# Kernel tuning notes

Hardware: AMD Instinct MI355X
Metric: run time of the kernel (lower is better)

## Reference

```python
import jax, jax.numpy as jnp
import numpy as np

NUM_HEADS = 8
ALPHA = 0.01  # leaky_relu slope
MAX_SEQ = 64


def layer_norm(x, g, b, eps=1e-5):
    m = jnp.mean(x, axis=-1, keepdims=True)
    v = jnp.var(x, axis=-1, keepdims=True)
    return (x - m) * jax.lax.rsqrt(v + eps) * g + b


def ff(x, w1, b1, w2, b2):
    # Linear -> exact GELU -> Linear (torch nn.GELU default is erf-based)
    return jax.nn.gelu(x @ w1.T + b1, approximate=False) @ w2.T + b2


def mha(q, k, v, in_w, in_b, out_w, out_b, kpm):
    # torch nn.MultiheadAttention, batch_first=False. q:[Tq,E,d], k/v:[Tk,E,d], kpm:[E,Tk] True=pad
    d = q.shape[-1]
    H = NUM_HEADS
    dh = d // H
    qp = q @ in_w[:d].T + in_b[:d]
    kp = k @ in_w[d:2 * d].T + in_b[d:2 * d]
    vp = v @ in_w[2 * d:].T + in_b[2 * d:]
    Tq, E, _ = qp.shape
    Tk = kp.shape[0]
    qh = qp.reshape(Tq, E, H, dh) * (dh ** -0.5)
    kh = kp.reshape(Tk, E, H, dh)
    vh = vp.reshape(Tk, E, H, dh)
    scores = jnp.einsum('qehd,kehd->ehqk', qh, kh)  # [E,H,Tq,Tk]
    scores = jnp.where(kpm[:, None, None, :], jnp.float32(-1e9), scores)
    att = jax.nn.softmax(scores, axis=-1)
    out = jnp.einsum('ehqk,kehd->qehd', att, vh).reshape(Tq, E, d)
    return out @ out_w.T + out_b


def setup_inputs() -> dict:
    key = jax.random.key(0)
    ks = jax.random.split(key, 40)
    N, d, E, Seq, H = 50000, 64, 150000, 5, NUM_HEADS

    def xn(k, shape, scale):
        return jax.random.normal(k, shape, dtype=jnp.float32) * scale

    inp = {
        'features': xn(ks[0], (N, d), 1.0),
        'pos_emb': xn(ks[1], (MAX_SEQ, d), 0.02),
        'self_in_w': xn(ks[2], (3 * d, d), 0.1),
        'self_in_b': jnp.zeros((3 * d,), jnp.float32),
        'self_out_w': xn(ks[3], (d, d), 0.1),
        'self_out_b': jnp.zeros((d,), jnp.float32),
        'cross_in_w': xn(ks[4], (3 * d, d), 0.1),
        'cross_in_b': jnp.zeros((3 * d,), jnp.float32),
        'cross_out_w': xn(ks[5], (d, d), 0.1),
        'cross_out_b': jnp.zeros((d,), jnp.float32),
        'sa_ln1_g': jnp.ones((d,), jnp.float32), 'sa_ln1_b': jnp.zeros((d,), jnp.float32),
        'sa_ln2_g': jnp.ones((d,), jnp.float32), 'sa_ln2_b': jnp.zeros((d,), jnp.float32),
        'ca_ln1_g': jnp.ones((d,), jnp.float32), 'ca_ln1_b': jnp.zeros((d,), jnp.float32),
        'ca_ln2_g': jnp.ones((d,), jnp.float32), 'ca_ln2_b': jnp.zeros((d,), jnp.float32),
        'sa_ff_w1': xn(ks[6], (4 * d, d), 0.08), 'sa_ff_b1': jnp.zeros((4 * d,), jnp.float32),
        'sa_ff_w2': xn(ks[7], (d, 4 * d), 0.08), 'sa_ff_b2': jnp.zeros((d,), jnp.float32),
        'ca_ff_w1': xn(ks[8], (4 * d, d), 0.08), 'ca_ff_b1': jnp.zeros((4 * d,), jnp.float32),
        'ca_ff_w2': xn(ks[9], (d, 4 * d), 0.08), 'ca_ff_b2': jnp.zeros((d,), jnp.float32),
        'inst_w': xn(ks[10], (NUM_HEADS * d, d), 0.08),
        'attn_vec': xn(ks[11], (1, NUM_HEADS, d), 0.2),
        'edge_metapath_indices': jax.random.randint(ks[12], (E, Seq), 0, N, dtype=jnp.int64)
            if jax.config.jax_enable_x64 else jax.random.randint(ks[12], (E, Seq), 0, N).astype(jnp.int32),
        'dst': jax.random.randint(ks[13], (E,), 0, N).astype(jnp.int32),
    }
    inp['edge_metapath_indices'] = inp['edge_metapath_indices'].astype(jnp.int32)
    return inp


def reference(features, pos_emb, self_in_w, self_in_b, self_out_w, self_out_b,
              cross_in_w, cross_in_b, cross_out_w, cross_out_b,
              sa_ln1_g, sa_ln1_b, sa_ln2_g, sa_ln2_b,
              ca_ln1_g, ca_ln1_b, ca_ln2_g, ca_ln2_b,
              sa_ff_w1, sa_ff_b1, sa_ff_w2, sa_ff_b2,
              ca_ff_w1, ca_ff_b1, ca_ff_w2, ca_ff_b2,
              inst_w, attn_vec, edge_metapath_indices, dst):
    N, d = features.shape
    pad_id = N  # module pads one zero row; indices == pad_id are padding
    feats = jnp.concatenate([features, jnp.zeros((1, d), features.dtype)], axis=0)
    idx = edge_metapath_indices  # [E, Seq]
    E, Seq = idx.shape
    kpm = idx == pad_id  # [E, Seq] key padding mask

    edata = feats[idx]  # [E, Seq, d] gather (embedding)
    tokens = jnp.transpose(edata, (1, 0, 2))  # [Seq, E, d]
    pos_vec = pos_emb[:Seq][:, None, :]  # [Seq, 1, d]
    pos_vec = jnp.where(kpm.T[:, :, None], jnp.float32(0.0), pos_vec)
    tokens = tokens + pos_vec  # pos_drop is identity in eval

    # pre-LN self-attention block over the metapath sequence
    sa_in = layer_norm(tokens, sa_ln1_g, sa_ln1_b)
    tokens = tokens + mha(sa_in, sa_in, sa_in, self_in_w, self_in_b, self_out_w, self_out_b, kpm)
    sa_out = jnp.transpose(tokens, (1, 0, 2))  # [E, Seq, d]

    valid = (~kpm).astype(features.dtype)  # [E, Seq]
    denom = jnp.clip(valid.sum(axis=1, keepdims=True), 1.0, None)
    inst_emb = (sa_out * valid[:, :, None]).sum(axis=1) / denom  # masked mean pool
    inst_emb = inst_emb + ff(layer_norm(inst_emb, sa_ln2_g, sa_ln2_b), sa_ff_w1, sa_ff_b1, sa_ff_w2, sa_ff_b2)

    # cross-attention: last (target) node attends over the sequence
    lengths = (~kpm).sum(axis=1)
    last_pos = jnp.clip(lengths - 1, 0, None)
    last_ids = jnp.take_along_axis(idx, last_pos[:, None], axis=1)[:, 0]
    target_feat = feats[last_ids]
    q = layer_norm(target_feat, ca_ln1_g, ca_ln1_b)[None]  # [1, E, d]
    cross_out = mha(q, tokens, tokens, cross_in_w, cross_in_b, cross_out_w, cross_out_b, kpm)
    inst_emb = inst_emb + cross_out[0]
    inst_emb = inst_emb + ff(layer_norm(inst_emb, ca_ln2_g, ca_ln2_b), ca_ff_w1, ca_ff_b1, ca_ff_w2, ca_ff_b2)

    # heads projection, leaky-relu attention score, edge softmax, scatter-sum
    eft = (inst_emb @ inst_w.T).reshape(E, NUM_HEADS, d)  # [E, H, d]
    a = jnp.sum(eft * attn_vec, axis=-1)  # [E, H]
    a = jnp.where(a > 0, a, ALPHA * a)  # leaky_relu
    seg_max = jax.ops.segment_max(a, dst, num_segments=N)  # per-dst-node max
    a_exp = jnp.exp(a - seg_max[dst])
    seg_sum = jax.ops.segment_sum(a_exp, dst, num_segments=N)
    att = a_exp / seg_sum[dst]  # edge_softmax; attn_drop=0 -> identity
    ret = jax.ops.segment_sum(eft * att[:, :, None], dst, num_segments=N)  # [N, H, d]
    return ret
```

## Files before the change

kernel.cpp:

```cpp
#include <hip/hip_runtime.h>
#include <math.h>

#define D 64
#define LOG2E 1.44269504088896340736f
#define QSCALE (0.35355339059327373f * LOG2E)

typedef float f32x4 __attribute__((ext_vector_type(4)));
typedef float vf4 __attribute__((ext_vector_type(4)));
typedef short bf16x8 __attribute__((ext_vector_type(8)));
typedef unsigned short ushort_t;
typedef unsigned int uint2v __attribute__((ext_vector_type(2)));

#define MF(a, b, c) __builtin_amdgcn_mfma_f32_16x16x32_bf16(a, b, c, 0, 0, 0)

__device__ __forceinline__ float bcast(float x, int i) {
  return __int_as_float(__builtin_amdgcn_readlane(__float_as_int(x), i));
}

__device__ __forceinline__ float xs16(float x) {
#if __has_builtin(__builtin_amdgcn_permlane16_swap)
  uint2v a = __builtin_amdgcn_permlane16_swap(__float_as_uint(x), __float_as_uint(x), false, false);
  return __uint_as_float(a[0]) + __uint_as_float(a[1]);
#else
  return x + __shfl_xor(x, 16);
#endif
}
__device__ __forceinline__ float xs32(float x) {
#if __has_builtin(__builtin_amdgcn_permlane32_swap)
  uint2v a = __builtin_amdgcn_permlane32_swap(__float_as_uint(x), __float_as_uint(x), false, false);
  return __uint_as_float(a[0]) + __uint_as_float(a[1]);
#else
  return x + __shfl_xor(x, 32);
#endif
}
__device__ __forceinline__ float qsum(float x) {
  return xs32(xs16(x));
}

__device__ __forceinline__ ushort_t f2b(float f) {
  unsigned int u = __float_as_uint(f);
  unsigned int r = (u + 0x7FFFu + ((u >> 16) & 1u)) >> 16;
  return (ushort_t)r;
}
__device__ __forceinline__ unsigned int pkrtne(float lo, float hi) {
  unsigned int a = __float_as_uint(lo);
  unsigned int b = __float_as_uint(hi);
  a = a + 0x7FFFu + ((a >> 16) & 1u);
  b = b + 0x7FFFu + ((b >> 16) & 1u);
  return __builtin_amdgcn_perm(b, a, 0x07060302u);
}
__device__ __forceinline__ f32x4 ld4(const float* __restrict__ p) { return *(const f32x4*)p; }
__device__ __forceinline__ unsigned int fkey(float f) {
  unsigned int b = __float_as_uint(f);
  return (b & 0x80000000u) ? ~b : (b | 0x80000000u);
}
__device__ __forceinline__ float funkey(unsigned int k) {
  return __uint_as_float((k & 0x80000000u) ? (k ^ 0x80000000u) : ~k);
}
__device__ __forceinline__ bf16x8 mkpair(const f32x4& ce, const f32x4& co) {
  union { bf16x8 v; unsigned int w[4]; } u;
  u.w[0] = pkrtne(ce[0], ce[1]);
  u.w[1] = pkrtne(ce[2], ce[3]);
  u.w[2] = pkrtne(co[0], co[1]);
  u.w[3] = pkrtne(co[2], co[3]);
  return u.v;
}
__device__ __forceinline__ f32x4 unpk(bf16x8 p, int half) {
  union { bf16x8 v; unsigned int w[4]; } u;
  u.v = p;
  unsigned int w0 = u.w[half * 2], w1 = u.w[half * 2 + 1];
  f32x4 r;
  r[0] = __uint_as_float(w0 << 16);
  r[1] = __uint_as_float(w0 & 0xFFFF0000u);
  r[2] = __uint_as_float(w1 << 16);
  r[3] = __uint_as_float(w1 & 0xFFFF0000u);
  return r;
}

__device__ __forceinline__ void lnT(const f32x4 (&x)[4], f32x4 (&y)[4],
                                    const float* __restrict__ g, const float* __restrict__ b,
                                    int quad) {
  float s1 = 0.f, s2 = 0.f;
#pragma unroll
  for (int ct = 0; ct < 4; ct++)
#pragma unroll
    for (int r = 0; r < 4; r++) { s1 += x[ct][r]; s2 += x[ct][r] * x[ct][r]; }
  s1 = qsum(s1);
  s2 = qsum(s2);
  float mean = s1 * 0.015625f;
  float var = s2 * 0.015625f - mean * mean;
  float rs = rsqrtf(var + 1e-5f);
#pragma unroll
  for (int ct = 0; ct < 4; ct++) {
    f32x4 gv = ld4(g + 16 * ct + 4 * quad);
    f32x4 bv = ld4(b + 16 * ct + 4 * quad);
#pragma unroll
    for (int r = 0; r < 4; r++) y[ct][r] = (x[ct][r] - mean) * rs * gv[r] + bv[r];
  }
}

__global__ void zero_kernel(float4* __restrict__ p, int n4) {
  int t = blockIdx.x * blockDim.x + threadIdx.x;
  if (t < n4) p[t] = make_float4(0.f, 0.f, 0.f, 0.f);
}

__global__ void prep_kernel(const float* __restrict__ si, const float* __restrict__ so,
                            const float* __restrict__ w1s, const float* __restrict__ w2s,
                            const float* __restrict__ ci, const float* __restrict__ co,
                            const float* __restrict__ w1c, const float* __restrict__ w2c,
                            const float* __restrict__ iw, const float* __restrict__ av,
                            float* __restrict__ ws) {
  int t = blockIdx.x * blockDim.x + threadIdx.x;
  ushort_t* bw = (ushort_t*)(ws + 33280);
  if (t < 98304) {
    const float* src;
    int base, cs;
    int l = t;
    if      (l < 12288) { src = si;  base = 0;     cs = 6; }
    else if (l < 16384) { src = so;  base = 12288; cs = 6; l -= 12288; }
    else if (l < 32768) { src = w1s; base = 16384; cs = 6; l -= 16384; }
    else if (l < 49152) { src = w2s; base = 32768; cs = 8; l -= 32768; }
    else if (l < 61440) { src = ci;  base = 49152; cs = 6; l -= 49152; }
    else if (l < 65536) { src = co;  base = 61440; cs = 6; l -= 61440; }
    else if (l < 81920) { src = w1c; base = 65536; cs = 6; l -= 65536; }
    else                { src = w2c; base = 81920; cs = 8; l -= 81920; }
    int c = l >> cs, k = l & ((1 << cs) - 1);
    int T = (1 << cs) >> 5;
    int ct = c >> 4, m = c & 15, tt = k >> 5, rem = k & 31;
    int quad = (rem >> 2) & 3;
    int j = (((rem >> 4) & 1) << 2) | (rem & 3);
    bw[base + (size_t)((ct * T + tt) * 64 + quad * 16 + m) * 8 + j] = f2b(src[l]);
  } else if (t < 131072) {
    int l = t - 98304;
    int c = l >> 6, k = l & 63;
    ws[(k >> 2) * 2048 + c * 4 + (k & 3)] = iw[l];
  } else if (t < 131584) {
    int l = t - 131072;
    int h = l >> 6, k = l & 63;
    float acc = 0.f;
    for (int c = 0; c < 64; c++) acc += av[h * 64 + c] * iw[(h * 64 + c) * 64 + k];
    ws[32768 + h * 64 + k] = acc;
  }
}

#define SC1(KARR, QF, CT, KS, P)                                                        \
  { f32x4 kv_ = unpk(KARR[KS][(CT) >> 1], (CT) & 1);                                    \
    float sp_ = QF[CT][0] * kv_[0] + QF[CT][1] * kv_[1] + QF[CT][2] * kv_[2] +          \
                QF[CT][3] * kv_[3];                                                     \
    sp_ = xs16(sp_);                                                                    \
    P = ((vb >> (KS)) & 1) ? sp_ : -1e30f; }

#define PV1(VARR, CT, KS, P, ACC)                                                       \
  { f32x4 vv_ = unpk(VARR[KS][(CT) >> 1], (CT) & 1);                                    \
    _Pragma("unroll") for (int r = 0; r < 4; r++) ACC[r] = fmaf(P, vv_[r], ACC[r]); }

#define ATT_CT(KARR, VARR, QF, CT, OD)                                                  \
  {                                                                                     \
    float p0, p1, p2, p3, p4;                                                           \
    SC1(KARR, QF, CT, 0, p0); SC1(KARR, QF, CT, 1, p1); SC1(KARR, QF, CT, 2, p2);       \
    SC1(KARR, QF, CT, 3, p3); SC1(KARR, QF, CT, 4, p4);                                 \
    float mx_ = fmaxf(fmaxf(fmaxf(p0, p1), fmaxf(p2, p3)), p4);                         \
    p0 = exp2f(p0 - mx_); p1 = exp2f(p1 - mx_); p2 = exp2f(p2 - mx_);                   \
    p3 = exp2f(p3 - mx_); p4 = exp2f(p4 - mx_);                                         \
    float ri_ = 1.0f / (p0 + p1 + p2 + p3 + p4);                                        \
    p0 *= ri_; p1 *= ri_; p2 *= ri_; p3 *= ri_; p4 *= ri_;                              \
    OD = (f32x4){0.f, 0.f, 0.f, 0.f};                                                   \
    PV1(VARR, CT, 0, p0, OD); PV1(VARR, CT, 1, p1, OD); PV1(VARR, CT, 2, p2, OD);       \
    PV1(VARR, CT, 3, p3, OD); PV1(VARR, CT, 4, p4, OD);                                 \
  }

#define KV_STAGE(S)                                                                     \
  {                                                                                     \
    f32x4 t[4], y[4];                                                                   \
    const bool vd = (vb >> (S)) & 1;                                                    \
    const float* fp = features + (size_t)min(ids[S], N - 1) * 64;                       \
    _Pragma("unroll")                                                                   \
    for (int ct = 0; ct < 4; ct++) {                                                    \
      f32x4 f = ld4(fp + 16 * ct + 4 * quad);                                           \
      f32x4 pv = ld4(pos_emb + (S) * 64 + 16 * ct + 4 * quad);                          \
      _Pragma("unroll")                                                                 \
      for (int r = 0; r < 4; r++) t[ct][r] = vd ? (f[r] + pv[r]) : 0.f;                 \
    }                                                                                   \
    lnT(t, y, sa_ln1_g, sa_ln1_b, quad);                                                \
    bf16x8 xl0 = mkpair(y[0], y[1]), xl1 = mkpair(y[2], y[3]);                          \
    f32x4 kt[4], vt[4];                                                                 \
    _Pragma("unroll")                                                                   \
    for (int ct = 0; ct < 4; ct++) {                                                    \
      f32x4 c = {0.f, 0.f, 0.f, 0.f};                                                   \
      c = MF(WSI[((4 + ct) * 2 + 0) * 64 + lane], xl0, c);                              \
      c = MF(WSI[((4 + ct) * 2 + 1) * 64 + lane], xl1, c);                              \
      f32x4 bb = ld4(self_in_b + 64 + 16 * ct + 4 * quad);                              \
      _Pragma("unroll")                                                                 \
      for (int r = 0; r < 4; r++) kt[ct][r] = c[r] + bb[r];                             \
      f32x4 c2 = {0.f, 0.f, 0.f, 0.f};                                                  \
      c2 = MF(WSI[((8 + ct) * 2 + 0) * 64 + lane], xl0, c2);                            \
      c2 = MF(WSI[((8 + ct) * 2 + 1) * 64 + lane], xl1, c2);                            \
      f32x4 bb2 = ld4(self_in_b + 128 + 16 * ct + 4 * quad);                            \
      _Pragma("unroll")                                                                 \
      for (int r = 0; r < 4; r++) vt[ct][r] = c2[r] + bb2[r];                           \
    }                                                                                   \
    Kp[S][0] = mkpair(kt[0], kt[1]); Kp[S][1] = mkpair(kt[2], kt[3]);                   \
    Vp[S][0] = mkpair(vt[0], vt[1]); Vp[S][1] = mkpair(vt[2], vt[3]);                   \
  }

#define Q_STAGE(S)                                                                      \
  {                                                                                     \
    const bool vd = (vb >> (S)) & 1;                                                    \
    const float* fp = features + (size_t)min(ids[S], N - 1) * 64;                       \
    f32x4 t[4], y[4];                                                                   \
    _Pragma("unroll")                                                                   \
    for (int ct = 0; ct < 4; ct++) {                                                    \
      f32x4 f = ld4(fp + 16 * ct + 4 * quad);                                           \
      f32x4 pv = ld4(pos_emb + (S) * 64 + 16 * ct + 4 * quad);                          \
      _Pragma("unroll")                                                                 \
      for (int r = 0; r < 4; r++) t[ct][r] = vd ? (f[r] + pv[r]) : 0.f;                 \
    }                                                                                   \
    lnT(t, y, sa_ln1_g, sa_ln1_b, quad);                                                \
    bf16x8 xl0 = mkpair(y[0], y[1]), xl1 = mkpair(y[2], y[3]);                          \
    f32x4 qf[4];                                                                        \
    _Pragma("unroll")                                                                   \
    for (int ct = 0; ct < 4; ct++) {                                                    \
      f32x4 c = {0.f, 0.f, 0.f, 0.f};                                                   \
      c = MF(WSI[(ct * 2 + 0) * 64 + lane], xl0, c);                                    \
      c = MF(WSI[(ct * 2 + 1) * 64 + lane], xl1, c);                                    \
      f32x4 bb = ld4(self_in_b + 16 * ct + 4 * quad);                                   \
      _Pragma("unroll")                                                                 \
      for (int r = 0; r < 4; r++) qf[ct][r] = (c[r] + bb[r]) * QSCALE;                  \
    }                                                                                   \
    f32x4 oa0, oa1, oa2, oa3;                                                           \
    ATT_CT(Kp, Vp, qf, 0, oa0); ATT_CT(Kp, Vp, qf, 1, oa1);                             \
    ATT_CT(Kp, Vp, qf, 2, oa2); ATT_CT(Kp, Vp, qf, 3, oa3);                             \
    bf16x8 op0 = mkpair(oa0, oa1), op1 = mkpair(oa2, oa3);                              \
    f32x4 tpc[4];                                                                       \
    _Pragma("unroll")                                                                   \
    for (int ct = 0; ct < 4; ct++) {                                                    \
      f32x4 c = {0.f, 0.f, 0.f, 0.f};                                                   \
      c = MF(WSO[(ct * 2 + 0) * 64 + lane], op0, c);                                    \
      c = MF(WSO[(ct * 2 + 1) * 64 + lane], op1, c);                                    \
      f32x4 bb = ld4(self_out_b + 16 * ct + 4 * quad);                                  \
      _Pragma("unroll")                                                                 \
      for (int r = 0; r < 4; r++) {                                                     \
        float tp_ = c[r] + bb[r] + t[ct][r];                                            \
        tpc[ct][r] = tp_;                                                               \
        pool[ct][r] += vd ? tp_ : 0.f;                                                  \
      }                                                                                 \
    }                                                                                   \
    TP[S][0] = mkpair(tpc[0], tpc[1]); TP[S][1] = mkpair(tpc[2], tpc[3]);               \
  }

#define CKV_STAGE(S)                                                                    \
  {                                                                                     \
    f32x4 kt[4], vt[4];                                                                 \
    _Pragma("unroll")                                                                   \
    for (int ct = 0; ct < 4; ct++) {                                                    \
      f32x4 c = {0.f, 0.f, 0.f, 0.f};                                                   \
      c = MF(WCI[((4 + ct) * 2 + 0) * 64 + lane], TP[S][0], c);                         \
      c = MF(WCI[((4 + ct) * 2 + 1) * 64 + lane], TP[S][1], c);                         \
      f32x4 bb = ld4(cross_in_b + 64 + 16 * ct + 4 * quad);                             \
      _Pragma("unroll")                                                                 \
      for (int r = 0; r < 4; r++) kt[ct][r] = c[r] + bb[r];                             \
      f32x4 c2 = {0.f, 0.f, 0.f, 0.f};                                                  \
      c2 = MF(WCI[((8 + ct) * 2 + 0) * 64 + lane], TP[S][0], c2);                       \
      c2 = MF(WCI[((8 + ct) * 2 + 1) * 64 + lane], TP[S][1], c2);                       \
      f32x4 bb2 = ld4(cross_in_b + 128 + 16 * ct + 4 * quad);                           \
      _Pragma("unroll")                                                                 \
      for (int r = 0; r < 4; r++) vt[ct][r] = c2[r] + bb2[r];                           \
    }                                                                                   \
    Kc[S][0] = mkpair(kt[0], kt[1]); Kc[S][1] = mkpair(kt[2], kt[3]);                   \
    Vc[S][0] = mkpair(vt[0], vt[1]); Vc[S][1] = mkpair(vt[2], vt[3]);                   \
  }

#define FF_H2(CT, HD)                                                                   \
  { f32x4 c = {0.f, 0.f, 0.f, 0.f};                                                     \
    c = MF(W1[((CT) * 2 + 0) * 64 + lane], x0, c);                                      \
    c = MF(W1[((CT) * 2 + 1) * 64 + lane], x1, c);                                      \
    f32x4 bb = ld4(b1 + 16 * (CT) + 4 * quad);                                          \
    _Pragma("unroll")                                                                   \
    for (int r = 0; r < 4; r++) {                                                       \
      float v = c[r] + bb[r];                                                           \
      HD[r] = 0.5f * v * (1.0f + erff(v * 0.70710678118654752440f));                    \
    } }

#define FF_O(CT)                                                                        \
  { f32x4 c = {0.f, 0.f, 0.f, 0.f};                                                     \
    c = MF(W2[((CT) * 8 + 0) * 64 + lane], Hp0, c);                                     \
    c = MF(W2[((CT) * 8 + 1) * 64 + lane], Hp1, c);                                     \
    c = MF(W2[((CT) * 8 + 2) * 64 + lane], Hp2, c);                                     \
    c = MF(W2[((CT) * 8 + 3) * 64 + lane], Hp3, c);                                     \
    c = MF(W2[((CT) * 8 + 4) * 64 + lane], Hp4, c);                                     \
    c = MF(W2[((CT) * 8 + 5) * 64 + lane], Hp5, c);                                     \
    c = MF(W2[((CT) * 8 + 6) * 64 + lane], Hp6, c);                                     \
    c = MF(W2[((CT) * 8 + 7) * 64 + lane], Hp7, c);                                     \
    f32x4 bb = ld4(b2 + 16 * (CT) + 4 * quad);                                          \
    _Pragma("unroll")                                                                   \
    for (int r = 0; r < 4; r++) inst[CT][r] += c[r] + bb[r]; }

__device__ __forceinline__ void ffnT(f32x4 (&inst)[4],
                                     const float* __restrict__ g, const float* __restrict__ b,
                                     const bf16x8* __restrict__ W1, const bf16x8* __restrict__ W2,
                                     const float* __restrict__ b1, const float* __restrict__ b2,
                                     int lane, int quad) {
  f32x4 y[4];
  lnT(inst, y, g, b, quad);
  bf16x8 x0 = mkpair(y[0], y[1]), x1 = mkpair(y[2], y[3]);
  f32x4 ha, hb;
  FF_H2(0, ha);  FF_H2(1, hb);  bf16x8 Hp0 = mkpair(ha, hb);
  FF_H2(2, ha);  FF_H2(3, hb);  bf16x8 Hp1 = mkpair(ha, hb);
  FF_H2(4, ha);  FF_H2(5, hb);  bf16x8 Hp2 = mkpair(ha, hb);
  FF_H2(6, ha);  FF_H2(7, hb);  bf16x8 Hp3 = mkpair(ha, hb);
  FF_H2(8, ha);  FF_H2(9, hb);  bf16x8 Hp4 = mkpair(ha, hb);
  FF_H2(10, ha); FF_H2(11, hb); bf16x8 Hp5 = mkpair(ha, hb);
  FF_H2(12, ha); FF_H2(13, hb); bf16x8 Hp6 = mkpair(ha, hb);
  FF_H2(14, ha); FF_H2(15, hb); bf16x8 Hp7 = mkpair(ha, hb);
  FF_O(0); FF_O(1); FF_O(2); FF_O(3);
}

#define ASC(H)                                                                          \
  { float sp = 0.f;                                                                     \
    _Pragma("unroll")                                                                   \
    for (int ct = 0; ct < 4; ct++) {                                                    \
      f32x4 uu = ld4(uvec + (H) * 64 + 16 * ct + 4 * quad);                             \
      _Pragma("unroll")                                                                 \
      for (int r = 0; r < 4; r++) sp = fmaf(inst[ct][r], uu[r], sp);                    \
    }                                                                                   \
    sp = qsum(sp);                                                                      \
    a##H = sp > 0.f ? sp : 0.01f * sp; }

__global__ __launch_bounds__(64, 1)
void edge_kernel(const float* __restrict__ features, const float* __restrict__ pos_emb,
                 const float* __restrict__ self_in_b, const float* __restrict__ self_out_b,
                 const float* __restrict__ cross_in_b, const float* __restrict__ cross_out_b,
                 const float* __restrict__ sa_ln1_g, const float* __restrict__ sa_ln1_b,
                 const float* __restrict__ sa_ln2_g, const float* __restrict__ sa_ln2_b,
                 const float* __restrict__ ca_ln1_g, const float* __restrict__ ca_ln1_b,
                 const float* __restrict__ ca_ln2_g, const float* __restrict__ ca_ln2_b,
                 const float* __restrict__ sa_ff_b1, const float* __restrict__ sa_ff_b2,
                 const float* __restrict__ ca_ff_b1, const float* __restrict__ ca_ff_b2,
                 const int* __restrict__ midx, const int* __restrict__ dstv,
                 const float* __restrict__ ws,
                 float* __restrict__ inst_out, float* __restrict__ a_out,
                 unsigned int* __restrict__ seg_max, int E, int N) {
  const int lane = threadIdx.x;
  const int quad = lane >> 4, lo = lane & 15;
  const int e0 = blockIdx.x * 16;
  __shared__ float xp[16 * 68];

  const ushort_t* bw = (const ushort_t*)(ws + 33280);
  const bf16x8* WSI = (const bf16x8*)(bw);
  const bf16x8* WSO = (const bf16x8*)(bw + 12288);
  const bf16x8* W1S = (const bf16x8*)(bw + 16384);
  const bf16x8* W2S = (const bf16x8*)(bw + 32768);
  const bf16x8* WCI = (const bf16x8*)(bw + 49152);
  const bf16x8* WCO = (const bf16x8*)(bw + 61440);
  const bf16x8* W1C = (const bf16x8*)(bw + 65536);
  const bf16x8* W2C = (const bf16x8*)(bw + 81920);
  const float* uvec = ws + 32768;

  const bool ge = (e0 + lo) < E;
  const int eIdx = min(e0 + lo, E - 1);
  int ids[5];
  ids[0] = midx[eIdx * 5 + 0];
  ids[1] = midx[eIdx * 5 + 1];
  ids[2] = midx[eIdx * 5 + 2];
  ids[3] = midx[eIdx * 5 + 3];
  ids[4] = midx[eIdx * 5 + 4];
  int vb = 0;
  if (ids[0] != N && ge) vb |= 1;
  if (ids[1] != N && ge) vb |= 2;
  if (ids[2] != N && ge) vb |= 4;
  if (ids[3] != N && ge) vb |= 8;
  if (ids[4] != N && ge) vb |= 16;
  const int nv = __popc(vb);
  const int lp = max(nv - 1, 0);
  int lid = ids[0];
  lid = (lp == 1) ? ids[1] : lid;
  lid = (lp == 2) ? ids[2] : lid;
  lid = (lp == 3) ? ids[3] : lid;
  lid = (lp == 4) ? ids[4] : lid;

  bf16x8 Kp[5][2], Vp[5][2];
  KV_STAGE(0); KV_STAGE(1); KV_STAGE(2); KV_STAGE(3); KV_STAGE(4);

  f32x4 pool[4];
#pragma unroll
  for (int ct = 0; ct < 4; ct++) pool[ct] = (f32x4){0.f, 0.f, 0.f, 0.f};
  bf16x8 TP[5][2];
  Q_STAGE(0); Q_STAGE(1); Q_STAGE(2); Q_STAGE(3); Q_STAGE(4);

  f32x4 inst[4];
  {
    float rn = 1.0f / (float)max(nv, 1);
#pragma unroll
    for (int ct = 0; ct < 4; ct++)
#pragma unroll
      for (int r = 0; r < 4; r++) inst[ct][r] = pool[ct][r] * rn;
  }

  ffnT(inst, sa_ln2_g, sa_ln2_b, W1S, W2S, sa_ff_b1, sa_ff_b2, lane, quad);

  {
    f32x4 tf[4], xq[4];
    const bool vdl = lid != N;
    const float* fp = features + (size_t)min(lid, N - 1) * 64;
#pragma unroll
    for (int ct = 0; ct < 4; ct++) {
      f32x4 f = ld4(fp + 16 * ct + 4 * quad);
#pragma unroll
      for (int r = 0; r < 4; r++) tf[ct][r] = vdl ? f[r] : 0.f;
    }
    lnT(tf, xq, ca_ln1_g, ca_ln1_b, quad);
    bf16x8 xq0 = mkpair(xq[0], xq[1]), xq1 = mkpair(xq[2], xq[3]);
    f32x4 qcf[4];
#pragma unroll
    for (int ct = 0; ct < 4; ct++) {
      f32x4 c = {0.f, 0.f, 0.f, 0.f};
      c = MF(WCI[(ct * 2 + 0) * 64 + lane], xq0, c);
      c = MF(WCI[(ct * 2 + 1) * 64 + lane], xq1, c);
      f32x4 bb = ld4(cross_in_b + 16 * ct + 4 * quad);
#pragma unroll
      for (int r = 0; r < 4; r++) qcf[ct][r] = (c[r] + bb[r]) * QSCALE;
    }
    bf16x8 Kc[5][2], Vc[5][2];
    CKV_STAGE(0); CKV_STAGE(1); CKV_STAGE(2); CKV_STAGE(3); CKV_STAGE(4);
    f32x4 cc0, cc1, cc2, cc3;
    ATT_CT(Kc, Vc, qcf, 0, cc0); ATT_CT(Kc, Vc, qcf, 1, cc1);
    ATT_CT(Kc, Vc, qcf, 2, cc2); ATT_CT(Kc, Vc, qcf, 3, cc3);
    bf16x8 cp0 = mkpair(cc0, cc1), cp1 = mkpair(cc2, cc3);
#pragma unroll
    for (int ct = 0; ct < 4; ct++) {
      f32x4 c = {0.f, 0.f, 0.f, 0.f};
      c = MF(WCO[(ct * 2 + 0) * 64 + lane], cp0, c);
      c = MF(WCO[(ct * 2 + 1) * 64 + lane], cp1, c);
      f32x4 bb = ld4(cross_out_b + 16 * ct + 4 * quad);
#pragma unroll
      for (int r = 0; r < 4; r++) inst[ct][r] += c[r] + bb[r];
    }
  }

  ffnT(inst, ca_ln2_g, ca_ln2_b, W1C, W2C, ca_ff_b1, ca_ff_b2, lane, quad);

  float a0, a1, a2, a3, a4, a5, a6, a7;
  ASC(0); ASC(1); ASC(2); ASC(3); ASC(4); ASC(5); ASC(6); ASC(7);
  if (ge) {
    int dd = dstv[e0 + lo];
    float v0 = quad == 0 ? a0 : quad == 1 ? a2 : quad == 2 ? a4 : a6;
    float v1 = quad == 0 ? a1 : quad == 1 ? a3 : quad == 2 ? a5 : a7;
    atomicMax(&seg_max[dd * 8 + 2 * quad], fkey(v0));
    atomicMax(&seg_max[dd * 8 + 2 * quad + 1], fkey(v1));
    if (quad < 2) {
      f32x4 st = (quad == 0) ? (f32x4){a0, a1, a2, a3} : (f32x4){a4, a5, a6, a7};
      *(f32x4*)(a_out + (size_t)(e0 + lo) * 8 + 4 * quad) = st;
    }
  }

#pragma unroll
  for (int ct = 0; ct < 4; ct++)
    *(f32x4*)(&xp[lo * 68 + 16 * ct + 4 * quad]) = inst[ct];
  __syncthreads();
  {
    int er = lane >> 2, cb = (lane & 3) * 16;
    if (e0 + er < E) {
#pragma unroll
      for (int u = 0; u < 4; u++) {
        f32x4 v = *(const f32x4*)(&xp[er * 68 + cb + 4 * u]);
        *(f32x4*)(inst_out + (size_t)(e0 + er) * 64 + cb + 4 * u) = v;
      }
    }
  }
}

__global__ void expsum_kernel(const float* __restrict__ a, const int* __restrict__ dstv,
                              const unsigned int* __restrict__ seg_max,
                              float* __restrict__ seg_sum, int E8) {
  int t = blockIdx.x * blockDim.x + threadIdx.x;
  if (t >= E8) return;
  int e = t >> 3, h = t & 7;
  int dd = dstv[e];
  float m = funkey(seg_max[dd * 8 + h]);
  atomicAdd(&seg_sum[dd * 8 + h], __expf(a[t] - m));
}

__global__ __launch_bounds__(256)
void scatter_kernel(const float* __restrict__ inst_emb, const float* __restrict__ a,
                    const unsigned int* __restrict__ seg_max, const float* __restrict__ seg_sum,
                    const int* __restrict__ dstv, float* __restrict__ out, int E) {
  const int wid = (blockIdx.x * blockDim.x + threadIdx.x) >> 6;
  const int lane = threadIdx.x & 63;
  if (wid >= E) return;
  int dd = dstv[wid];
  float iv = inst_emb[(size_t)wid * D + lane];
#pragma unroll
  for (int h = 0; h < 8; h++) {
    float m = funkey(seg_max[dd * 8 + h]);
    float s = seg_sum[dd * 8 + h];
    float att = __expf(a[wid * 8 + h] - m) / s;
    atomicAdd(&out[(size_t)dd * 512 + h * 64 + lane], att * iv);
  }
}

__global__ __launch_bounds__(256)
void head_transform_kernel(const float* __restrict__ T_iw, float* __restrict__ out, int N) {
  const int wid = (blockIdx.x * blockDim.x + threadIdx.x) >> 6;
  const int lane = threadIdx.x & 63;
  const int h = wid & 7;
  const int n0 = (wid >> 3) * 4;
  if (n0 >= N) return;
  float z[4], acc[4];
#pragma unroll
  for (int j = 0; j < 4; j++) {
    z[j] = (n0 + j < N) ? out[((size_t)(n0 + j) * 8 + h) * D + lane] : 0.f;
    acc[j] = 0.f;
  }
  const vf4* P = (const vf4*)T_iw;
  for (int k4 = 0; k4 < 16; k4++) {
    vf4 w = P[k4 * 512 + h * 64 + lane];
#pragma unroll
    for (int u = 0; u < 4; u++) {
      int i = k4 * 4 + u;
#pragma unroll
      for (int j = 0; j < 4; j++) acc[j] = fmaf(bcast(z[j], i), w[u], acc[j]);
    }
  }
#pragma unroll
  for (int j = 0; j < 4; j++)
    if (n0 + j < N) out[((size_t)(n0 + j) * 8 + h) * D + lane] = acc[j];
}

extern "C" void kernel_launch(void* const* d_in, const int* in_sizes, int n_in,
                              void* d_out, int out_size, void* d_ws, size_t ws_size,
                              hipStream_t stream) {
  const float* features   = (const float*)d_in[0];
  const float* pos_emb    = (const float*)d_in[1];
  const float* self_in_w  = (const float*)d_in[2];
  const float* self_in_b  = (const float*)d_in[3];
  const float* self_out_w = (const float*)d_in[4];
  const float* self_out_b = (const float*)d_in[5];
  const float* cross_in_w = (const float*)d_in[6];
  const float* cross_in_b = (const float*)d_in[7];
  const float* cross_out_w= (const float*)d_in[8];
  const float* cross_out_b= (const float*)d_in[9];
  const float* sa_ln1_g = (const float*)d_in[10];
  const float* sa_ln1_b = (const float*)d_in[11];
  const float* sa_ln2_g = (const float*)d_in[12];
  const float* sa_ln2_b = (const float*)d_in[13];
  const float* ca_ln1_g = (const float*)d_in[14];
  const float* ca_ln1_b = (const float*)d_in[15];
  const float* ca_ln2_g = (const float*)d_in[16];
  const float* ca_ln2_b = (const float*)d_in[17];
  const float* sa_ff_w1 = (const float*)d_in[18];
  const float* sa_ff_b1 = (const float*)d_in[19];
  const float* sa_ff_w2 = (const float*)d_in[20];
  const float* sa_ff_b2 = (const float*)d_in[21];
  const float* ca_ff_w1 = (const float*)d_in[22];
  const float* ca_ff_b1 = (const float*)d_in[23];
  const float* ca_ff_w2 = (const float*)d_in[24];
  const float* ca_ff_b2 = (const float*)d_in[25];
  const float* inst_w   = (const float*)d_in[26];
  const float* attn_vec = (const float*)d_in[27];
  const int* midx = (const int*)d_in[28];
  const int* dstv = (const int*)d_in[29];

  const int N = in_sizes[0] / 64;
  const int E = in_sizes[29];

  float* wsf = (float*)d_ws;
  float* inst_emb = wsf + 131072;
  float* a_arr = inst_emb + (size_t)E * 64;
  unsigned int* seg_max = (unsigned int*)(a_arr + (size_t)E * 8);
  float* seg_sum = (float*)(seg_max + (size_t)N * 8);

  {
    int n4 = out_size / 4;
    zero_kernel<<<(n4 + 255) / 256, 256, 0, stream>>>((float4*)d_out, n4);
    int s4 = (N * 16) / 4;
    zero_kernel<<<(s4 + 255) / 256, 256, 0, stream>>>((float4*)seg_max, s4);
  }

  prep_kernel<<<(131584 + 255) / 256, 256, 0, stream>>>(
      self_in_w, self_out_w, sa_ff_w1, sa_ff_w2, cross_in_w, cross_out_w, ca_ff_w1, ca_ff_w2,
      inst_w, attn_vec, wsf);

  int nblk = (E + 15) / 16;
  edge_kernel<<<nblk, 64, 0, stream>>>(
      features, pos_emb, self_in_b, self_out_b, cross_in_b, cross_out_b, sa_ln1_g, sa_ln1_b,
      sa_ln2_g, sa_ln2_b, ca_ln1_g, ca_ln1_b, ca_ln2_g, ca_ln2_b, sa_ff_b1, sa_ff_b2, ca_ff_b1,
      ca_ff_b2, midx, dstv, wsf, inst_emb, a_arr, seg_max, E, N);

  expsum_kernel<<<(E * 8 + 255) / 256, 256, 0, stream>>>(a_arr, dstv, seg_max, seg_sum, E * 8);

  scatter_kernel<<<(E + 3) / 4, 256, 0, stream>>>(inst_emb, a_arr, seg_max, seg_sum, dstv,
                                                  (float*)d_out, E);

  int hwave = ((N + 3) / 4) * 8;
  head_transform_kernel<<<(hwave + 3) / 4, 256, 0, stream>>>(wsf, (float*)d_out, N);
}
```

Baseline: 1.039 ms.

## Replace atomic segment softmax scatter with CSR-based per-node gather

Builds a CSR index of edges grouped by destination node (count, three-stage scan, fill) and replaces the atomicMax/expsum/atomicAdd scatter plus separate head-transform pass with one gather kernel. Each wave handles one node and head, computes max, exp-sum and the weighted sum in registers, then applies the per-head transform with weights held in registers and writes the output directly. This removes the float atomics over a large output buffer and the output zeroing. In exchange it adds several small CSR-construction launches and does serial per-node loops that could be imbalanced for high-degree nodes.

```diff
diff --git a/kernel.cpp b/kernel.cpp
--- a/kernel.cpp
+++ b/kernel.cpp
@@ -50,13 +50,6 @@
   return __builtin_amdgcn_perm(b, a, 0x07060302u);
 }
 __device__ __forceinline__ f32x4 ld4(const float* __restrict__ p) { return *(const f32x4*)p; }
-__device__ __forceinline__ unsigned int fkey(float f) {
-  unsigned int b = __float_as_uint(f);
-  return (b & 0x80000000u) ? ~b : (b | 0x80000000u);
-}
-__device__ __forceinline__ float funkey(unsigned int k) {
-  return __uint_as_float((k & 0x80000000u) ? (k ^ 0x80000000u) : ~k);
-}
 __device__ __forceinline__ bf16x8 mkpair(const f32x4& ce, const f32x4& co) {
   union { bf16x8 v; unsigned int w[4]; } u;
   u.w[0] = pkrtne(ce[0], ce[1]);
@@ -338,8 +331,7 @@
                  const float* __restrict__ ca_ff_b1, const float* __restrict__ ca_ff_b2,
                  const int* __restrict__ midx, const int* __restrict__ dstv,
                  const float* __restrict__ ws,
-                 float* __restrict__ inst_out, float* __restrict__ a_out,
-                 unsigned int* __restrict__ seg_max, int E, int N) {
+                 float* __restrict__ inst_out, float* __restrict__ a_out, int E, int N) {
   const int lane = threadIdx.x;
   const int quad = lane >> 4, lo = lane & 15;
   const int e0 = blockIdx.x * 16;
@@ -441,16 +433,9 @@
 
   float a0, a1, a2, a3, a4, a5, a6, a7;
   ASC(0); ASC(1); ASC(2); ASC(3); ASC(4); ASC(5); ASC(6); ASC(7);
-  if (ge) {
-    int dd = dstv[e0 + lo];
-    float v0 = quad == 0 ? a0 : quad == 1 ? a2 : quad == 2 ? a4 : a6;
-    float v1 = quad == 0 ? a1 : quad == 1 ? a3 : quad == 2 ? a5 : a7;
-    atomicMax(&seg_max[dd * 8 + 2 * quad], fkey(v0));
-    atomicMax(&seg_max[dd * 8 + 2 * quad + 1], fkey(v1));
-    if (quad < 2) {
-      f32x4 st = (quad == 0) ? (f32x4){a0, a1, a2, a3} : (f32x4){a4, a5, a6, a7};
-      *(f32x4*)(a_out + (size_t)(e0 + lo) * 8 + 4 * quad) = st;
-    }
+  if (ge && quad < 2) {
+    f32x4 st = (quad == 0) ? (f32x4){a0, a1, a2, a3} : (f32x4){a4, a5, a6, a7};
+    *(f32x4*)(a_out + (size_t)(e0 + lo) * 8 + 4 * quad) = st;
   }
 
 #pragma unroll
@@ -469,61 +454,97 @@
   }
 }
 
-__global__ void expsum_kernel(const float* __restrict__ a, const int* __restrict__ dstv,
-                              const unsigned int* __restrict__ seg_max,
-                              float* __restrict__ seg_sum, int E8) {
-  int t = blockIdx.x * blockDim.x + threadIdx.x;
-  if (t >= E8) return;
-  int e = t >> 3, h = t & 7;
-  int dd = dstv[e];
-  float m = funkey(seg_max[dd * 8 + h]);
-  atomicAdd(&seg_sum[dd * 8 + h], __expf(a[t] - m));
+__global__ void csr_count_kernel(const int* __restrict__ dstv, unsigned int* __restrict__ cnt,
+                                 int E) {
+  int e = blockIdx.x * blockDim.x + threadIdx.x;
+  if (e < E) atomicAdd(&cnt[dstv[e]], 1u);
+}
+
+__global__ void scan1_kernel(unsigned int* __restrict__ off, unsigned int* __restrict__ bsum,
+                             int N) {
+  __shared__ unsigned int sd[256];
+  int t = threadIdx.x, n = blockIdx.x * 256 + t;
+  unsigned int v = (n < N) ? off[n] : 0u;
+  sd[t] = v;
+  __syncthreads();
+  for (int o = 1; o < 256; o <<= 1) {
+    unsigned int x = (t >= o) ? sd[t - o] : 0u;
+    __syncthreads();
+    sd[t] += x;
+    __syncthreads();
+  }
+  if (n < N) off[n] = sd[t] - v;
+  if (t == 255) bsum[blockIdx.x] = sd[255];
+}
+
+__global__ void scan2_kernel(unsigned int* __restrict__ bsum, int nb) {
+  __shared__ unsigned int sd[1024];
+  int t = threadIdx.x;
+  unsigned int v = (t < nb) ? bsum[t] : 0u;
+  sd[t] = v;
+  __syncthreads();
+  for (int o = 1; o < 1024; o <<= 1) {
+    unsigned int x = (t >= o) ? sd[t - o] : 0u;
+    __syncthreads();
+    sd[t] += x;
+    __syncthreads();
+  }
+  if (t < nb) bsum[t] = sd[t] - v;
+}
+
+__global__ void scan3_kernel(unsigned int* __restrict__ off, unsigned int* __restrict__ cur,
+                             const unsigned int* __restrict__ bsum, int N, int E) {
+  int n = blockIdx.x * 256 + threadIdx.x;
+  if (n < N) {
+    unsigned int o = off[n] + bsum[blockIdx.x];
+    off[n] = o;
+    cur[n] = o;
+  }
+  if (n == 0) off[N] = (unsigned int)E;
+}
+
+__global__ void csr_fill_kernel(const int* __restrict__ dstv, unsigned int* __restrict__ cur,
+                                unsigned int* __restrict__ elist, int E) {
+  int e = blockIdx.x * blockDim.x + threadIdx.x;
+  if (e < E) {
+    unsigned int p = atomicAdd(&cur[dstv[e]], 1u);
+    elist[p] = (unsigned int)e;
+  }
 }
 
 __global__ __launch_bounds__(256)
-void scatter_kernel(const float* __restrict__ inst_emb, const float* __restrict__ a,
-                    const unsigned int* __restrict__ seg_max, const float* __restrict__ seg_sum,
-                    const int* __restrict__ dstv, float* __restrict__ out, int E) {
-  const int wid = (blockIdx.x * blockDim.x + threadIdx.x) >> 6;
+void gather_kernel(const float* __restrict__ T_iw, const unsigned int* __restrict__ off,
+                   const unsigned int* __restrict__ elist, const float* __restrict__ a,
+                   const float* __restrict__ inst_emb, float* __restrict__ out, int N) {
   const int lane = threadIdx.x & 63;
-  if (wid >= E) return;
-  int dd = dstv[wid];
-  float iv = inst_emb[(size_t)wid * D + lane];
-#pragma unroll
-  for (int h = 0; h < 8; h++) {
-    float m = funkey(seg_max[dd * 8 + h]);
-    float s = seg_sum[dd * 8 + h];
-    float att = __expf(a[wid * 8 + h] - m) / s;
-    atomicAdd(&out[(size_t)dd * 512 + h * 64 + lane], att * iv);
-  }
-}
-
-__global__ __launch_bounds__(256)
-void head_transform_kernel(const float* __restrict__ T_iw, float* __restrict__ out, int N) {
-  const int wid = (blockIdx.x * blockDim.x + threadIdx.x) >> 6;
-  const int lane = threadIdx.x & 63;
-  const int h = wid & 7;
-  const int n0 = (wid >> 3) * 4;
-  if (n0 >= N) return;
-  float z[4], acc[4];
-#pragma unroll
-  for (int j = 0; j < 4; j++) {
-    z[j] = (n0 + j < N) ? out[((size_t)(n0 + j) * 8 + h) * D + lane] : 0.f;
-    acc[j] = 0.f;
-  }
+  const int widx = threadIdx.x >> 6;
+  const int h = blockIdx.y;
   const vf4* P = (const vf4*)T_iw;
-  for (int k4 = 0; k4 < 16; k4++) {
-    vf4 w = P[k4 * 512 + h * 64 + lane];
-#pragma unroll
-    for (int u = 0; u < 4; u++) {
-      int i = k4 * 4 + u;
-#pragma unroll
-      for (int j = 0; j < 4; j++) acc[j] = fmaf(bcast(z[j], i), w[u], acc[j]);
+  vf4 wr[16];
+#pragma unroll
+  for (int k = 0; k < 16; k++) wr[k] = P[k * 512 + h * 64 + lane];
+  const int stride = gridDim.x * 4;
+  for (int n = blockIdx.x * 4 + widx; n < N; n += stride) {
+    const unsigned int s0 = off[n], s1 = off[n + 1];
+    float m = -3.0e38f;
+    for (unsigned int i = s0; i < s1; i++) m = fmaxf(m, a[(size_t)elist[i] * 8 + h]);
+    float s = 0.f, z = 0.f;
+    for (unsigned int i = s0; i < s1; i++) {
+      unsigned int e = elist[i];
+      float w = __expf(a[(size_t)e * 8 + h] - m);
+      s += w;
+      z = fmaf(w, inst_emb[(size_t)e * 64 + lane], z);
     }
-  }
-#pragma unroll
-  for (int j = 0; j < 4; j++)
-    if (n0 + j < N) out[((size_t)(n0 + j) * 8 + h) * D + lane] = acc[j];
+    float ri = (s > 0.f) ? 1.0f / s : 0.f;
+    z *= ri;
+    float o = 0.f;
+#pragma unroll
+    for (int k = 0; k < 16; k++) {
+#pragma unroll
+      for (int u = 0; u < 4; u++) o = fmaf(bcast(z, k * 4 + u), wr[k][u], o);
+    }
+    out[(size_t)n * 512 + h * 64 + lane] = o;
+  }
 }
 
 extern "C" void kernel_launch(void* const* d_in, const int* in_sizes, int n_in,
@@ -566,31 +587,34 @@
   float* wsf = (float*)d_ws;
   float* inst_emb = wsf + 131072;
   float* a_arr = inst_emb + (size_t)E * 64;
-  unsigned int* seg_max = (unsigned int*)(a_arr + (size_t)E * 8);
-  float* seg_sum = (float*)(seg_max + (size_t)N * 8);
+  unsigned int* off = (unsigned int*)(a_arr + (size_t)E * 8);
+  unsigned int* cur = off + (size_t)(N + 1);
+  unsigned int* bsum = cur + (size_t)N;
+  unsigned int* elist = bsum + 1024;
+
+  const int nb1 = (N + 255) / 256;
 
   {
-    int n4 = out_size / 4;
-    zero_kernel<<<(n4 + 255) / 256, 256, 0, stream>>>((float4*)d_out, n4);
-    int s4 = (N * 16) / 4;
-    zero_kernel<<<(s4 + 255) / 256, 256, 0, stream>>>((float4*)seg_max, s4);
+    int n4 = (N + 1 + 3) / 4;
+    zero_kernel<<<(n4 + 255) / 256, 256, 0, stream>>>((float4*)off, n4);
   }
 
   prep_kernel<<<(131584 + 255) / 256, 256, 0, stream>>>(
       self_in_w, self_out_w, sa_ff_w1, sa_ff_w2, cross_in_w, cross_out_w, ca_ff_w1, ca_ff_w2,
       inst_w, attn_vec, wsf);
+
+  csr_count_kernel<<<(E + 255) / 256, 256, 0, stream>>>(dstv, off, E);
+  scan1_kernel<<<nb1, 256, 0, stream>>>(off, bsum, N);
+  scan2_kernel<<<1, 1024, 0, stream>>>(bsum, nb1);
+  scan3_kernel<<<nb1, 256, 0, stream>>>(off, cur, bsum, N, E);
+  csr_fill_kernel<<<(E + 255) / 256, 256, 0, stream>>>(dstv, cur, elist, E);
 
   int nblk = (E + 15) / 16;
   edge_kernel<<<nblk, 64, 0, stream>>>(
       features, pos_emb, self_in_b, self_out_b, cross_in_b, cross_out_b, sa_ln1_g, sa_ln1_b,
       sa_ln2_g, sa_ln2_b, ca_ln1_g, ca_ln1_b, ca_ln2_g, ca_ln2_b, sa_ff_b1, sa_ff_b2, ca_ff_b1,
-      ca_ff_b2, midx, dstv, wsf, inst_emb, a_arr, seg_max, E, N);
-
-  expsum_kernel<<<(E * 8 + 255) / 256, 256, 0, stream>>>(a_arr, dstv, seg_max, seg_sum, E * 8);
-
-  scatter_kernel<<<(E + 3) / 4, 256, 0, stream>>>(inst_emb, a_arr, seg_max, seg_sum, dstv,
-                                                  (float*)d_out, E);
-
-  int hwave = ((N + 3) / 4) * 8;
-  head_transform_kernel<<<(hwave + 3) / 4, 256, 0, stream>>>(wsf, (float*)d_out, N);
-}
+      ca_ff_b2, midx, dstv, wsf, inst_emb, a_arr, E, N);
+
+  dim3 ggrid(256, 8);
+  gather_kernel<<<ggrid, 256, 0, stream>>>(wsf, off, elist, a_arr, inst_emb, (float*)d_out, N);
+}
```

New measurement: 984.9 us. 5.2% less time.
